# Optimization experiments

Measured on AMD Instinct MI355X. Metric: run time of the kernel, lower is better.

Reference implementation:

```python
import jax, jax.numpy as jnp
import numpy as np

B, L, D, H, NL, EXP = 8, 1024, 512, 8, 6, 4
DH = D // H
DF = D * EXP
EPS = 1e-3  # keras LayerNormalization default epsilon
NEG = -1e9  # keras Softmax mask adder for float32


def _ln(x, g, b):
    m = jnp.mean(x, axis=-1, keepdims=True)
    v = jnp.mean(jnp.square(x - m), axis=-1, keepdims=True)
    return (x - m) * jax.lax.rsqrt(v + EPS) * g + b


def _pos_emb(L, D):
    pos = jnp.arange(L, dtype=jnp.float32)[:, None]          # [L,1]
    i = jnp.arange(D // 2, dtype=jnp.float32)[None, :]        # [1,D/2]
    inv = jnp.power(10000.0, -2.0 * i / D)
    # original concatenates sin block then cos block along feature axis
    return jnp.concatenate([jnp.sin(pos * inv), jnp.cos(pos * inv)], axis=-1)  # [L,D]


def setup_inputs() -> dict:
    key = jax.random.key(0)
    ks = jax.random.split(key, 16)
    glorot = lambda k, shape: jax.random.uniform(
        k, shape, jnp.float32, -1.0, 1.0) * jnp.sqrt(6.0 / (shape[-2] + shape[-1]))
    return {
        "x": jax.random.normal(ks[0], (B, L, D), jnp.float32),
        "lengths": jax.random.randint(ks[1], (B,), L // 2, L + 1).astype(jnp.int32),
        "Wq": glorot(ks[2], (NL, D, D)),
        "Wk": glorot(ks[3], (NL, D, D)),
        "Wv": glorot(ks[4], (NL, D, D)),
        "Wo": glorot(ks[5], (NL, D, D)),
        "ln1_g": jnp.ones((NL, D), jnp.float32),
        "ln1_b": jnp.zeros((NL, D), jnp.float32),
        "ln2_g": jnp.ones((NL, D), jnp.float32),
        "ln2_b": jnp.zeros((NL, D), jnp.float32),
        "w1": glorot(ks[6], (NL, D, DF)),
        "b1": jnp.zeros((NL, DF), jnp.float32),
        "w2": glorot(ks[7], (NL, DF, D)),
        "b2": jnp.zeros((NL, D), jnp.float32),
    }


def _forward(x, mask_bias, Wq, Wk, Wv, Wo, ln1_g, ln1_b, ln2_g, ln2_b, w1, b1, w2, b2):
    x = x + _pos_emb(L, D)[None, :, :]
    scale = 1.0 / jnp.sqrt(jnp.float32(DH))

    def layer(x, p):
        wq, wk, wv, wo, g1, be1, g2, be2, fw1, fb1, fw2, fb2 = p
        h = _ln(x, g1, be1)
        split = lambda t: t.reshape(B, L, H, DH).transpose(0, 2, 1, 3)  # [B,H,L,DH]
        q, k, v = split(h @ wq), split(h @ wk), split(h @ wv)
        scores = jnp.einsum("bhqd,bhkd->bhqk", q, k) * scale + mask_bias
        attn = jax.nn.softmax(scores, axis=-1)
        o = jnp.einsum("bhqk,bhkd->bhqd", attn, v)
        o = o.transpose(0, 2, 1, 3).reshape(B, L, D) @ wo
        x = x + o  # dropout is identity at inference
        h2 = _ln(x, g2, be2)
        ffn = jax.nn.relu(h2 @ fw1 + fb1) @ fw2 + fb2
        return x + ffn, None

    x, _ = jax.lax.scan(layer, x, (Wq, Wk, Wv, Wo, ln1_g, ln1_b, ln2_g, ln2_b, w1, b1, w2, b2))
    return x


def reference(x, lengths, Wq, Wk, Wv, Wo, ln1_g, ln1_b, ln2_g, ln2_b, w1, b1, w2, b2):
    mask = (jnp.arange(L)[None, :] < lengths[:, None]).astype(jnp.float32)  # [B,L]
    mask_bias = (1.0 - mask)[:, None, None, :] * NEG                        # [B,1,1,L]
    return _forward(x, mask_bias, Wq, Wk, Wv, Wo, ln1_g, ln1_b, ln2_g, ln2_b, w1, b1, w2, b2)
```

## Files before the change

### kernel.cpp

```cpp
#include <hip/hip_runtime.h>
#include <cstdint>
#include <cstddef>

#define Bz 8
#define Lz 1024
#define Dz 512
#define Hz 8
#define NLz 6
#define DFz 2048
#define Mz (Bz*Lz)

typedef short bf16x8 __attribute__((ext_vector_type(8)));
typedef float f32x4  __attribute__((ext_vector_type(4)));

__device__ __forceinline__ short f2bf(float f) {
    unsigned u = __builtin_bit_cast(unsigned, f);
    u = (u + 0x7fff + ((u >> 16) & 1)) >> 16;
    return (short)u;
}

__device__ __forceinline__ float exp2_fast(float x) {
#if __has_builtin(__builtin_amdgcn_exp2f)
    return __builtin_amdgcn_exp2f(x);
#else
    return exp2f(x);
#endif
}

#define GLD16(gp, lp) __builtin_amdgcn_global_load_lds( \
    (const __attribute__((address_space(1))) void*)(gp), \
    (__attribute__((address_space(3))) void*)(lp), 16, 0, 0)

__global__ __launch_bounds__(256) void posadd_kernel(const float* __restrict__ x,
                                                     float* __restrict__ y) {
    int idx = blockIdx.x * 256 + threadIdx.x;
    int d   = idx & (Dz - 1);
    int pos = (idx >> 9) & (Lz - 1);
    int i2  = (d < Dz/2) ? d : d - Dz/2;
    float inv = __expf(-0.03597789207f * (float)i2);
    float a = (float)pos * inv;
    float pe = (d < Dz/2) ? sinf(a) : cosf(a);
    y[idx] = x[idx] + pe;
}

__global__ __launch_bounds__(256) void ln_kernel(const float* __restrict__ x,
                                                 const float* __restrict__ g,
                                                 const float* __restrict__ b,
                                                 short* __restrict__ out) {
    int row = blockIdx.x;
    int t = threadIdx.x;
    const float* xr = x + (size_t)row * Dz;
    float v0 = xr[t], v1 = xr[t + 256];
    float s = v0 + v1;
    #pragma unroll
    for (int off = 32; off; off >>= 1) s += __shfl_xor(s, off, 64);
    __shared__ float red[4];
    int w = t >> 6, l = t & 63;
    if (l == 0) red[w] = s;
    __syncthreads();
    float m = (red[0] + red[1] + red[2] + red[3]) * (1.0f / Dz);
    float d0 = v0 - m, d1 = v1 - m;
    float s2 = d0 * d0 + d1 * d1;
    #pragma unroll
    for (int off = 32; off; off >>= 1) s2 += __shfl_xor(s2, off, 64);
    __syncthreads();
    if (l == 0) red[w] = s2;
    __syncthreads();
    float var = (red[0] + red[1] + red[2] + red[3]) * (1.0f / Dz);
    float rs = rsqrtf(var + 1e-3f);
    out[(size_t)row * Dz + t]       = f2bf(d0 * rs * g[t] + b[t]);
    out[(size_t)row * Dz + t + 256] = f2bf(d1 * rs * g[t + 256] + b[t + 256]);
}

__global__ __launch_bounds__(256) void transpose_bf16_kernel(const float* __restrict__ src,
                                                             short* __restrict__ dst,
                                                             int K, int N,
                                                             long srcLS, long dstLS, int rowOff) {
    __shared__ float tile[32][33];
    int tx = threadIdx.x & 31, ty = threadIdx.x >> 5;
    int bx = blockIdx.x, by = blockIdx.y, z = blockIdx.z;
    const float* s = src + (size_t)z * srcLS;
    short* d = dst + (size_t)z * dstLS;
    #pragma unroll
    for (int i = 0; i < 4; i++)
        tile[ty + i * 8][tx] = s[(size_t)(by * 32 + ty + i * 8) * N + bx * 32 + tx];
    __syncthreads();
    #pragma unroll
    for (int i = 0; i < 4; i++)
        d[(size_t)(rowOff + bx * 32 + ty + i * 8) * K + by * 32 + tx] = f2bf(tile[tx][ty + i * 8]);
}

__global__ __launch_bounds__(256) void vtrans_kernel(const short* __restrict__ qkv,
                                                     short* __restrict__ vbt) {
    int lt = blockIdx.x, bh = blockIdx.y;
    int b = bh >> 3, h = bh & 7;
    __shared__ short tile[64][72];
    int t = threadIdx.x;
    int l = t >> 2, c4 = t & 3;
    #pragma unroll
    for (int p = 0; p < 2; p++) {
        int dd = (c4 + p * 4) * 8;
        *(uint4*)&tile[l][dd] =
            *(const uint4*)(qkv + ((size_t)(b * Lz + lt * 64 + l)) * 1536 + 1024 + h * 64 + dd);
    }
    __syncthreads();
    int d = t >> 2;
    #pragma unroll
    for (int p = 0; p < 2; p++) {
        int lc = (c4 + p * 4) * 8;
        union { uint4 u; short s[8]; } o;
        #pragma unroll
        for (int j = 0; j < 8; j++) o.s[j] = tile[lc + j][d];
        *(uint4*)(vbt + ((size_t)(bh * 64 + d)) * Lz + lt * 64 + lc) = o.u;
    }
}

template<int MODE, int TN>
__global__ __launch_bounds__(256, (TN == 64) ? 4 : 2)
void gemm_bt(const short* __restrict__ A,
             const short* __restrict__ Bt,
             short* __restrict__ outb,
             float* __restrict__ outf,
             const float* __restrict__ bias,
             int M, int N, int K) {
    constexpr int NI = TN / 32;
    __shared__ __attribute__((aligned(16))) short As[128 * 32];
    __shared__ __attribute__((aligned(16))) short Bs[TN * 32];
    int t = threadIdx.x;
    int m0 = blockIdx.x * 128, n0 = blockIdx.y * TN;
    int w = t >> 6, l = t & 63;
    int wm = (w >> 1) * 64, wn = (w & 1) * (TN / 2);
    int lr = l & 15, lq = l >> 4;
    f32x4 acc[4][NI] = {};
    int ra0 = t >> 2, ca0 = (t & 3) * 8;
    int ra1 = (t + 256) >> 2;
    for (int kk = 0; kk < K; kk += 32) {
        GLD16(A + (size_t)(m0 + ra0) * K + kk + ca0, As + t * 8);
        GLD16(A + (size_t)(m0 + ra1) * K + kk + ca0, As + (t + 256) * 8);
        GLD16(Bt + (size_t)(n0 + ra0) * K + kk + ca0, Bs + t * 8);
        if constexpr (TN == 128)
            GLD16(Bt + (size_t)(n0 + ra1) * K + kk + ca0, Bs + (t + 256) * 8);
        __syncthreads();
        bf16x8 af[4], bfr[NI];
        #pragma unroll
        for (int i = 0; i < 4; i++)  af[i]  = *(const bf16x8*)(As + (wm + i * 16 + lr) * 32 + lq * 8);
        #pragma unroll
        for (int i = 0; i < NI; i++) bfr[i] = *(const bf16x8*)(Bs + (wn + i * 16 + lr) * 32 + lq * 8);
        #pragma unroll
        for (int mi = 0; mi < 4; mi++)
            #pragma unroll
            for (int ni = 0; ni < NI; ni++)
                acc[mi][ni] = __builtin_amdgcn_mfma_f32_16x16x32_bf16(af[mi], bfr[ni], acc[mi][ni], 0, 0, 0);
        __syncthreads();
    }
    #pragma unroll
    for (int mi = 0; mi < 4; mi++)
        #pragma unroll
        for (int ni = 0; ni < NI; ni++) {
            int col = n0 + wn + ni * 16 + lr;
            float bv = (MODE == 2 || MODE == 3) ? bias[col] : 0.0f;
            #pragma unroll
            for (int r = 0; r < 4; r++) {
                int row = m0 + wm + mi * 16 + lq * 4 + r;
                size_t idx = (size_t)row * N + col;
                float v = acc[mi][ni][r];
                if (MODE == 0)      outb[idx] = f2bf(v);
                else if (MODE == 1) outf[idx] += v;
                else if (MODE == 2) outb[idx] = f2bf(fmaxf(v + bv, 0.0f));
                else                outf[idx] += v + bv;
            }
        }
}

__device__ __forceinline__ void attn_frag(f32x4* sacc, const float* biask,
                                          float* mr, float* lsum, f32x4* oacc,
                                          short* Pw, const short* Vs,
                                          int lr, int lq, bf16x8 onesf) {
    const float SC2 = 0.18033688f;
    float p[8][4];
    #pragma unroll
    for (int r = 0; r < 4; r++) {
        float mx = -1e30f;
        #pragma unroll
        for (int kt = 0; kt < 8; kt++) {
            p[kt][r] = sacc[kt][r] * SC2 + biask[kt];
            mx = fmaxf(mx, p[kt][r]);
        }
        mx = fmaxf(mx, __shfl_xor(mx, 1, 64));
        mx = fmaxf(mx, __shfl_xor(mx, 2, 64));
        mx = fmaxf(mx, __shfl_xor(mx, 4, 64));
        mx = fmaxf(mx, __shfl_xor(mx, 8, 64));
        float mn = fmaxf(mr[r], mx);
        float alpha = exp2_fast(mr[r] - mn);
        mr[r] = mn;
        #pragma unroll
        for (int kt = 0; kt < 8; kt++)
            p[kt][r] = exp2_fast(p[kt][r] - mn);
        lsum[r] *= alpha;
        #pragma unroll
        for (int ni = 0; ni < 4; ni++) oacc[ni][r] *= alpha;
    }
    #pragma unroll
    for (int kt = 0; kt < 8; kt++)
        #pragma unroll
        for (int r = 0; r < 4; r++)
            Pw[(lq * 4 + r) * 136 + kt * 16 + lr] = f2bf(p[kt][r]);
    f32x4 sums = {};
    #pragma unroll
    for (int c = 0; c < 4; c++) {
        bf16x8 pf = *(const bf16x8*)(Pw + lr * 136 + c * 32 + lq * 8);
        sums = __builtin_amdgcn_mfma_f32_16x16x32_bf16(pf, onesf, sums, 0, 0, 0);
        #pragma unroll
        for (int ni = 0; ni < 4; ni++) {
            bf16x8 vf = *(const bf16x8*)(Vs + (ni * 16 + lr) * 136 + c * 32 + lq * 8);
            oacc[ni] = __builtin_amdgcn_mfma_f32_16x16x32_bf16(pf, vf, oacc[ni], 0, 0, 0);
        }
    }
    #pragma unroll
    for (int r = 0; r < 4; r++) lsum[r] += sums[r];
}

__global__ __launch_bounds__(256, 2) void attn_kernel(const short* __restrict__ qkv,
                                                      const short* __restrict__ vbt,
                                                      const int* __restrict__ lengths,
                                                      short* __restrict__ o) {
    __shared__ __attribute__((aligned(16))) short Ks[128 * 72];
    __shared__ __attribute__((aligned(16))) short Vs[64 * 136];
    __shared__ __attribute__((aligned(16))) short Ps[4][16 * 136];
    int qt = blockIdx.x;
    int bh = blockIdx.y;
    int b = bh >> 3, h = bh & 7;
    int len = lengths[b];
    int t = threadIdx.x, w = t >> 6, l = t & 63;
    int lr = l & 15, lq = l >> 4;

    const short* q0 = qkv + (size_t)(b * Lz + qt * 128 + w * 32 + lr) * 1536 + h * 64 + lq * 8;
    bf16x8 qf0a = *(const bf16x8*)(q0);
    bf16x8 qf0b = *(const bf16x8*)(q0 + 32);
    bf16x8 qf1a = *(const bf16x8*)(q0 + 16 * 1536);
    bf16x8 qf1b = *(const bf16x8*)(q0 + 16 * 1536 + 32);

    int kkey = t >> 3, kd8 = (t & 7) * 8;
    int vd = t >> 4, vk8 = (t & 15) * 8;
    const short* kbaseg = qkv + (size_t)(b * Lz) * 1536 + 512 + h * 64;
    const short* vbaseg = vbt + (size_t)(bh * 64) * Lz;

    float mr0[4] = {-1e30f, -1e30f, -1e30f, -1e30f}, ls0[4] = {0.f, 0.f, 0.f, 0.f};
    float mr1[4] = {-1e30f, -1e30f, -1e30f, -1e30f}, ls1[4] = {0.f, 0.f, 0.f, 0.f};
    f32x4 oacc0[4] = {}, oacc1[4] = {};
    bf16x8 onesf = {0x3F80, 0x3F80, 0x3F80, 0x3F80, 0x3F80, 0x3F80, 0x3F80, 0x3F80};

    uint4 kreg[4], vreg[4];
    #pragma unroll
    for (int i = 0; i < 4; i++)
        kreg[i] = *(const uint4*)(kbaseg + (size_t)(i * 32 + kkey) * 1536 + kd8);

    short* Pw = &Ps[w][0];
    int ntiles = (len + 127) >> 7;
    for (int tix = 0; tix < ntiles; tix++) {
        int k0 = tix << 7;
        __syncthreads();
        #pragma unroll
        for (int i = 0; i < 4; i++)
            *(uint4*)(Ks + (i * 32 + kkey) * 72 + kd8) = kreg[i];
        __syncthreads();
        #pragma unroll
        for (int i = 0; i < 4; i++)
            vreg[i] = *(const uint4*)(vbaseg + (size_t)(i * 16 + vd) * Lz + k0 + vk8);
        f32x4 sacc[8] = {};
        #pragma unroll
        for (int kt = 0; kt < 8; kt++) {
            bf16x8 kf0 = *(const bf16x8*)(Ks + (kt * 16 + lr) * 72 + lq * 8);
            bf16x8 kf1 = *(const bf16x8*)(Ks + (kt * 16 + lr) * 72 + 32 + lq * 8);
            sacc[kt] = __builtin_amdgcn_mfma_f32_16x16x32_bf16(qf0a, kf0, sacc[kt], 0, 0, 0);
            sacc[kt] = __builtin_amdgcn_mfma_f32_16x16x32_bf16(qf0b, kf1, sacc[kt], 0, 0, 0);
        }
        if (tix + 1 < ntiles) {
            #pragma unroll
            for (int i = 0; i < 4; i++)
                kreg[i] = *(const uint4*)(kbaseg + (size_t)(k0 + 128 + i * 32 + kkey) * 1536 + kd8);
        }
        #pragma unroll
        for (int i = 0; i < 4; i++)
            *(uint4*)(Vs + (i * 16 + vd) * 136 + vk8) = vreg[i];
        float biask[8];
        #pragma unroll
        for (int kt = 0; kt < 8; kt++)
            biask[kt] = ((k0 + kt * 16 + lr) < len) ? 0.0f : -1e30f;
        __syncthreads();
        attn_frag(sacc, biask, mr0, ls0, oacc0, Pw, Vs, lr, lq, onesf);
        #pragma unroll
        for (int kt = 0; kt < 8; kt++) {
            bf16x8 kf0 = *(const bf16x8*)(Ks + (kt * 16 + lr) * 72 + lq * 8);
            bf16x8 kf1 = *(const bf16x8*)(Ks + (kt * 16 + lr) * 72 + 32 + lq * 8);
            f32x4 s2 = {};
            s2 = __builtin_amdgcn_mfma_f32_16x16x32_bf16(qf1a, kf0, s2, 0, 0, 0);
            s2 = __builtin_amdgcn_mfma_f32_16x16x32_bf16(qf1b, kf1, s2, 0, 0, 0);
            sacc[kt] = s2;
        }
        attn_frag(sacc, biask, mr1, ls1, oacc1, Pw, Vs, lr, lq, onesf);
    }
    #pragma unroll
    for (int ni = 0; ni < 4; ni++)
        #pragma unroll
        for (int r = 0; r < 4; r++) {
            int q = qt * 128 + w * 32 + lq * 4 + r;
            size_t base = (size_t)(b * Lz + q) * Dz + h * 64 + ni * 16 + lr;
            o[base]             = f2bf(oacc0[ni][r] / ls0[r]);
            o[base + 16 * Dz]   = f2bf(oacc1[ni][r] / ls1[r]);
        }
}

extern "C" void kernel_launch(void* const* d_in, const int* in_sizes, int n_in,
                              void* d_out, int out_size, void* d_ws, size_t ws_size,
                              hipStream_t stream) {
    const float* x_in    = (const float*)d_in[0];
    const int*   lengths = (const int*)d_in[1];
    const float* Wq   = (const float*)d_in[2];
    const float* Wk   = (const float*)d_in[3];
    const float* Wv   = (const float*)d_in[4];
    const float* Wo   = (const float*)d_in[5];
    const float* ln1g = (const float*)d_in[6];
    const float* ln1b = (const float*)d_in[7];
    const float* ln2g = (const float*)d_in[8];
    const float* ln2b = (const float*)d_in[9];
    const float* w1   = (const float*)d_in[10];
    const float* b1   = (const float*)d_in[11];
    const float* w2   = (const float*)d_in[12];
    const float* b2   = (const float*)d_in[13];

    size_t off = 0;
    auto alloc = [&](size_t bytes) {
        void* p = (char*)d_ws + off;
        off += (bytes + 255) & ~(size_t)255;
        return p;
    };
    float* x_work = (float*)alloc((size_t)Mz * Dz * 4);
    short* hbuf   = (short*)alloc((size_t)Mz * Dz * 2);
    short* qkvb   = (short*)alloc((size_t)Mz * 1536 * 2);
    short* f1b    = (short*)alloc((size_t)Mz * DFz * 2);
    short* vbt    = (short*)alloc((size_t)Bz * Hz * 64 * Lz * 2);
    short* wqkvT  = (short*)alloc((size_t)NLz * 1536 * Dz * 2);
    short* woT    = (short*)alloc((size_t)NLz * Dz * Dz * 2);
    short* w1T    = (short*)alloc((size_t)NLz * DFz * Dz * 2);
    short* w2T    = (short*)alloc((size_t)NLz * Dz * DFz * 2);

    dim3 tb(256);
    transpose_bf16_kernel<<<dim3(16, 16, NLz), tb, 0, stream>>>(Wq, wqkvT, Dz, Dz, (long)Dz*Dz, (long)1536*Dz, 0);
    transpose_bf16_kernel<<<dim3(16, 16, NLz), tb, 0, stream>>>(Wk, wqkvT, Dz, Dz, (long)Dz*Dz, (long)1536*Dz, 512);
    transpose_bf16_kernel<<<dim3(16, 16, NLz), tb, 0, stream>>>(Wv, wqkvT, Dz, Dz, (long)Dz*Dz, (long)1536*Dz, 1024);
    transpose_bf16_kernel<<<dim3(16, 16, NLz), tb, 0, stream>>>(Wo, woT, Dz, Dz, (long)Dz*Dz, (long)Dz*Dz, 0);
    transpose_bf16_kernel<<<dim3(64, 16, NLz), tb, 0, stream>>>(w1, w1T, Dz, DFz, (long)Dz*DFz, (long)DFz*Dz, 0);
    transpose_bf16_kernel<<<dim3(16, 64, NLz), tb, 0, stream>>>(w2, w2T, DFz, Dz, (long)DFz*Dz, (long)Dz*DFz, 0);

    posadd_kernel<<<dim3(Mz * Dz / 256), tb, 0, stream>>>(x_in, x_work);

    for (int lyr = 0; lyr < NLz; lyr++) {
        const short* wqkvL = wqkvT + (size_t)lyr * 1536 * Dz;
        const short* woL   = woT   + (size_t)lyr * Dz * Dz;
        const short* w1L   = w1T   + (size_t)lyr * DFz * Dz;
        const short* w2L   = w2T   + (size_t)lyr * Dz * DFz;

        ln_kernel<<<dim3(Mz), tb, 0, stream>>>(x_work, ln1g + lyr * Dz, ln1b + lyr * Dz, hbuf);
        gemm_bt<0,128><<<dim3(Mz/128, 1536/128), tb, 0, stream>>>(hbuf, wqkvL, qkvb, nullptr, nullptr, Mz, 1536, Dz);
        vtrans_kernel<<<dim3(Lz/64, Bz*Hz), tb, 0, stream>>>(qkvb, vbt);
        attn_kernel<<<dim3(Lz/128, Bz*Hz), tb, 0, stream>>>(qkvb, vbt, lengths, hbuf);
        gemm_bt<1,64><<<dim3(Mz/128, Dz/64), tb, 0, stream>>>(hbuf, woL, nullptr, x_work, nullptr, Mz, Dz, Dz);
        ln_kernel<<<dim3(Mz), tb, 0, stream>>>(x_work, ln2g + lyr * Dz, ln2b + lyr * Dz, hbuf);
        gemm_bt<2,128><<<dim3(Mz/128, DFz/128), tb, 0, stream>>>(hbuf, w1L, f1b, nullptr, b1 + lyr * DFz, Mz, DFz, Dz);
        gemm_bt<3,64><<<dim3(Mz/128, Dz/64), tb, 0, stream>>>(f1b, w2L, nullptr, x_work, b2 + lyr * Dz, Mz, Dz, DFz);
    }

    hipMemcpyAsync(d_out, x_work, (size_t)Mz * Dz * 4, hipMemcpyDeviceToDevice, stream);
}
```

Baseline: 1.195 ms.

## Use 8 waves per attention block with one 16-row query slice each

The attention kernel moves from 256 threads handling two 16-row query fragments per wave to 512 threads with one fragment per wave, and the helper function is inlined. K and V tiles for the next key block are both prefetched into registers before the current block's compute, which removes one barrier per tile. MFMA sections are wrapped in s_setprio to favour matrix issue. The aim is more waves in flight to hide latency and lower register pressure per wave, at the cost of more LDS for P buffers and more threads sharing each K/V tile.

```diff
diff --git a/kernel.cpp b/kernel.cpp
--- a/kernel.cpp
+++ b/kernel.cpp
@@ -172,88 +172,41 @@
         }
 }
 
-__device__ __forceinline__ void attn_frag(f32x4* sacc, const float* biask,
-                                          float* mr, float* lsum, f32x4* oacc,
-                                          short* Pw, const short* Vs,
-                                          int lr, int lq, bf16x8 onesf) {
-    const float SC2 = 0.18033688f;
-    float p[8][4];
-    #pragma unroll
-    for (int r = 0; r < 4; r++) {
-        float mx = -1e30f;
-        #pragma unroll
-        for (int kt = 0; kt < 8; kt++) {
-            p[kt][r] = sacc[kt][r] * SC2 + biask[kt];
-            mx = fmaxf(mx, p[kt][r]);
-        }
-        mx = fmaxf(mx, __shfl_xor(mx, 1, 64));
-        mx = fmaxf(mx, __shfl_xor(mx, 2, 64));
-        mx = fmaxf(mx, __shfl_xor(mx, 4, 64));
-        mx = fmaxf(mx, __shfl_xor(mx, 8, 64));
-        float mn = fmaxf(mr[r], mx);
-        float alpha = exp2_fast(mr[r] - mn);
-        mr[r] = mn;
-        #pragma unroll
-        for (int kt = 0; kt < 8; kt++)
-            p[kt][r] = exp2_fast(p[kt][r] - mn);
-        lsum[r] *= alpha;
-        #pragma unroll
-        for (int ni = 0; ni < 4; ni++) oacc[ni][r] *= alpha;
-    }
-    #pragma unroll
-    for (int kt = 0; kt < 8; kt++)
-        #pragma unroll
-        for (int r = 0; r < 4; r++)
-            Pw[(lq * 4 + r) * 136 + kt * 16 + lr] = f2bf(p[kt][r]);
-    f32x4 sums = {};
-    #pragma unroll
-    for (int c = 0; c < 4; c++) {
-        bf16x8 pf = *(const bf16x8*)(Pw + lr * 136 + c * 32 + lq * 8);
-        sums = __builtin_amdgcn_mfma_f32_16x16x32_bf16(pf, onesf, sums, 0, 0, 0);
-        #pragma unroll
-        for (int ni = 0; ni < 4; ni++) {
-            bf16x8 vf = *(const bf16x8*)(Vs + (ni * 16 + lr) * 136 + c * 32 + lq * 8);
-            oacc[ni] = __builtin_amdgcn_mfma_f32_16x16x32_bf16(pf, vf, oacc[ni], 0, 0, 0);
-        }
-    }
-    #pragma unroll
-    for (int r = 0; r < 4; r++) lsum[r] += sums[r];
-}
-
-__global__ __launch_bounds__(256, 2) void attn_kernel(const short* __restrict__ qkv,
+__global__ __launch_bounds__(512, 4) void attn_kernel(const short* __restrict__ qkv,
                                                       const short* __restrict__ vbt,
                                                       const int* __restrict__ lengths,
                                                       short* __restrict__ o) {
     __shared__ __attribute__((aligned(16))) short Ks[128 * 72];
     __shared__ __attribute__((aligned(16))) short Vs[64 * 136];
-    __shared__ __attribute__((aligned(16))) short Ps[4][16 * 136];
+    __shared__ __attribute__((aligned(16))) short Ps[8][16 * 136];
     int qt = blockIdx.x;
     int bh = blockIdx.y;
     int b = bh >> 3, h = bh & 7;
     int len = lengths[b];
     int t = threadIdx.x, w = t >> 6, l = t & 63;
     int lr = l & 15, lq = l >> 4;
-
-    const short* q0 = qkv + (size_t)(b * Lz + qt * 128 + w * 32 + lr) * 1536 + h * 64 + lq * 8;
-    bf16x8 qf0a = *(const bf16x8*)(q0);
-    bf16x8 qf0b = *(const bf16x8*)(q0 + 32);
-    bf16x8 qf1a = *(const bf16x8*)(q0 + 16 * 1536);
-    bf16x8 qf1b = *(const bf16x8*)(q0 + 16 * 1536 + 32);
+    const float SC2 = 0.18033688f;
+
+    const short* q0 = qkv + (size_t)(b * Lz + qt * 128 + w * 16 + lr) * 1536 + h * 64 + lq * 8;
+    bf16x8 qfa = *(const bf16x8*)(q0);
+    bf16x8 qfb = *(const bf16x8*)(q0 + 32);
 
     int kkey = t >> 3, kd8 = (t & 7) * 8;
     int vd = t >> 4, vk8 = (t & 15) * 8;
     const short* kbaseg = qkv + (size_t)(b * Lz) * 1536 + 512 + h * 64;
     const short* vbaseg = vbt + (size_t)(bh * 64) * Lz;
 
-    float mr0[4] = {-1e30f, -1e30f, -1e30f, -1e30f}, ls0[4] = {0.f, 0.f, 0.f, 0.f};
-    float mr1[4] = {-1e30f, -1e30f, -1e30f, -1e30f}, ls1[4] = {0.f, 0.f, 0.f, 0.f};
-    f32x4 oacc0[4] = {}, oacc1[4] = {};
+    float mr[4] = {-1e30f, -1e30f, -1e30f, -1e30f}, ls[4] = {0.f, 0.f, 0.f, 0.f};
+    f32x4 oacc[4] = {};
     bf16x8 onesf = {0x3F80, 0x3F80, 0x3F80, 0x3F80, 0x3F80, 0x3F80, 0x3F80, 0x3F80};
 
-    uint4 kreg[4], vreg[4];
-    #pragma unroll
-    for (int i = 0; i < 4; i++)
-        kreg[i] = *(const uint4*)(kbaseg + (size_t)(i * 32 + kkey) * 1536 + kd8);
+    uint4 kreg[2], vreg[2];
+    #pragma unroll
+    for (int i = 0; i < 2; i++)
+        kreg[i] = *(const uint4*)(kbaseg + (size_t)(i * 64 + kkey) * 1536 + kd8);
+    #pragma unroll
+    for (int i = 0; i < 2; i++)
+        vreg[i] = *(const uint4*)(vbaseg + (size_t)(i * 32 + vd) * Lz + vk8);
 
     short* Pw = &Ps[w][0];
     int ntiles = (len + 127) >> 7;
@@ -261,53 +214,83 @@
         int k0 = tix << 7;
         __syncthreads();
         #pragma unroll
-        for (int i = 0; i < 4; i++)
-            *(uint4*)(Ks + (i * 32 + kkey) * 72 + kd8) = kreg[i];
+        for (int i = 0; i < 2; i++)
+            *(uint4*)(Ks + (i * 64 + kkey) * 72 + kd8) = kreg[i];
+        #pragma unroll
+        for (int i = 0; i < 2; i++)
+            *(uint4*)(Vs + (i * 32 + vd) * 136 + vk8) = vreg[i];
         __syncthreads();
-        #pragma unroll
-        for (int i = 0; i < 4; i++)
-            vreg[i] = *(const uint4*)(vbaseg + (size_t)(i * 16 + vd) * Lz + k0 + vk8);
+        if (tix + 1 < ntiles) {
+            int kn = k0 + 128;
+            #pragma unroll
+            for (int i = 0; i < 2; i++)
+                kreg[i] = *(const uint4*)(kbaseg + (size_t)(kn + i * 64 + kkey) * 1536 + kd8);
+            #pragma unroll
+            for (int i = 0; i < 2; i++)
+                vreg[i] = *(const uint4*)(vbaseg + (size_t)(i * 32 + vd) * Lz + kn + vk8);
+        }
         f32x4 sacc[8] = {};
+        __builtin_amdgcn_s_setprio(1);
         #pragma unroll
         for (int kt = 0; kt < 8; kt++) {
             bf16x8 kf0 = *(const bf16x8*)(Ks + (kt * 16 + lr) * 72 + lq * 8);
             bf16x8 kf1 = *(const bf16x8*)(Ks + (kt * 16 + lr) * 72 + 32 + lq * 8);
-            sacc[kt] = __builtin_amdgcn_mfma_f32_16x16x32_bf16(qf0a, kf0, sacc[kt], 0, 0, 0);
-            sacc[kt] = __builtin_amdgcn_mfma_f32_16x16x32_bf16(qf0b, kf1, sacc[kt], 0, 0, 0);
-        }
-        if (tix + 1 < ntiles) {
-            #pragma unroll
-            for (int i = 0; i < 4; i++)
-                kreg[i] = *(const uint4*)(kbaseg + (size_t)(k0 + 128 + i * 32 + kkey) * 1536 + kd8);
-        }
-        #pragma unroll
-        for (int i = 0; i < 4; i++)
-            *(uint4*)(Vs + (i * 16 + vd) * 136 + vk8) = vreg[i];
-        float biask[8];
+            sacc[kt] = __builtin_amdgcn_mfma_f32_16x16x32_bf16(qfa, kf0, sacc[kt], 0, 0, 0);
+            sacc[kt] = __builtin_amdgcn_mfma_f32_16x16x32_bf16(qfb, kf1, sacc[kt], 0, 0, 0);
+        }
+        __builtin_amdgcn_s_setprio(0);
+        #pragma unroll
+        for (int r = 0; r < 4; r++) {
+            float mx = -1e30f;
+            #pragma unroll
+            for (int kt = 0; kt < 8; kt++) {
+                float bv = ((k0 + kt * 16 + lr) < len) ? 0.0f : -1e30f;
+                float v = sacc[kt][r] * SC2 + bv;
+                sacc[kt][r] = v;
+                mx = fmaxf(mx, v);
+            }
+            mx = fmaxf(mx, __shfl_xor(mx, 1, 64));
+            mx = fmaxf(mx, __shfl_xor(mx, 2, 64));
+            mx = fmaxf(mx, __shfl_xor(mx, 4, 64));
+            mx = fmaxf(mx, __shfl_xor(mx, 8, 64));
+            float mn = fmaxf(mr[r], mx);
+            float alpha = exp2_fast(mr[r] - mn);
+            mr[r] = mn;
+            #pragma unroll
+            for (int kt = 0; kt < 8; kt++)
+                sacc[kt][r] = exp2_fast(sacc[kt][r] - mn);
+            ls[r] *= alpha;
+            #pragma unroll
+            for (int ni = 0; ni < 4; ni++) oacc[ni][r] *= alpha;
+        }
         #pragma unroll
         for (int kt = 0; kt < 8; kt++)
-            biask[kt] = ((k0 + kt * 16 + lr) < len) ? 0.0f : -1e30f;
-        __syncthreads();
-        attn_frag(sacc, biask, mr0, ls0, oacc0, Pw, Vs, lr, lq, onesf);
-        #pragma unroll
-        for (int kt = 0; kt < 8; kt++) {
-            bf16x8 kf0 = *(const bf16x8*)(Ks + (kt * 16 + lr) * 72 + lq * 8);
-            bf16x8 kf1 = *(const bf16x8*)(Ks + (kt * 16 + lr) * 72 + 32 + lq * 8);
-            f32x4 s2 = {};
-            s2 = __builtin_amdgcn_mfma_f32_16x16x32_bf16(qf1a, kf0, s2, 0, 0, 0);
-            s2 = __builtin_amdgcn_mfma_f32_16x16x32_bf16(qf1b, kf1, s2, 0, 0, 0);
-            sacc[kt] = s2;
-        }
-        attn_frag(sacc, biask, mr1, ls1, oacc1, Pw, Vs, lr, lq, onesf);
+            #pragma unroll
+            for (int r = 0; r < 4; r++)
+                Pw[(lq * 4 + r) * 136 + kt * 16 + lr] = f2bf(sacc[kt][r]);
+        f32x4 sums = {};
+        __builtin_amdgcn_s_setprio(1);
+        #pragma unroll
+        for (int c = 0; c < 4; c++) {
+            bf16x8 pf = *(const bf16x8*)(Pw + lr * 136 + c * 32 + lq * 8);
+            sums = __builtin_amdgcn_mfma_f32_16x16x32_bf16(pf, onesf, sums, 0, 0, 0);
+            #pragma unroll
+            for (int ni = 0; ni < 4; ni++) {
+                bf16x8 vf = *(const bf16x8*)(Vs + (ni * 16 + lr) * 136 + c * 32 + lq * 8);
+                oacc[ni] = __builtin_amdgcn_mfma_f32_16x16x32_bf16(pf, vf, oacc[ni], 0, 0, 0);
+            }
+        }
+        __builtin_amdgcn_s_setprio(0);
+        #pragma unroll
+        for (int r = 0; r < 4; r++) ls[r] += sums[r];
     }
     #pragma unroll
     for (int ni = 0; ni < 4; ni++)
         #pragma unroll
         for (int r = 0; r < 4; r++) {
-            int q = qt * 128 + w * 32 + lq * 4 + r;
+            int q = qt * 128 + w * 16 + lq * 4 + r;
             size_t base = (size_t)(b * Lz + q) * Dz + h * 64 + ni * 16 + lr;
-            o[base]             = f2bf(oacc0[ni][r] / ls0[r]);
-            o[base + 16 * Dz]   = f2bf(oacc1[ni][r] / ls1[r]);
+            o[base] = f2bf(oacc[ni][r] / ls[r]);
         }
 }
 
@@ -364,7 +347,7 @@
         ln_kernel<<<dim3(Mz), tb, 0, stream>>>(x_work, ln1g + lyr * Dz, ln1b + lyr * Dz, hbuf);
         gemm_bt<0,128><<<dim3(Mz/128, 1536/128), tb, 0, stream>>>(hbuf, wqkvL, qkvb, nullptr, nullptr, Mz, 1536, Dz);
         vtrans_kernel<<<dim3(Lz/64, Bz*Hz), tb, 0, stream>>>(qkvb, vbt);
-        attn_kernel<<<dim3(Lz/128, Bz*Hz), tb, 0, stream>>>(qkvb, vbt, lengths, hbuf);
+        attn_kernel<<<dim3(Lz/128, Bz*Hz), dim3(512), 0, stream>>>(qkvb, vbt, lengths, hbuf);
         gemm_bt<1,64><<<dim3(Mz/128, Dz/64), tb, 0, stream>>>(hbuf, woL, nullptr, x_work, nullptr, Mz, Dz, Dz);
         ln_kernel<<<dim3(Mz), tb, 0, stream>>>(x_work, ln2g + lyr * Dz, ln2b + lyr * Dz, hbuf);
         gemm_bt<2,128><<<dim3(Mz/128, DFz/128), tb, 0, stream>>>(hbuf, w1L, f1b, nullptr, b1 + lyr * DFz, Mz, DFz, Dz);
```

After: 1.250 ms. +4.6%, slower.
